# Optimization experiments

Hardware: AMD Instinct MI355X
Metric: run time of the kernel (lower is better)

The kernel has to match this reference:

```python
import jax, jax.numpy as jnp
import numpy as np

# Module hyperparameters (init_kwargs): d_in=256, d_out=512, nh=8 -> dv=dk=dd=64
D_IN, D_OUT, NH = 256, 512, 8
DV = D_OUT // NH   # 64
DK = DV            # 64
DD = DK            # 64
KH, KW = 3, 7
D_HID = NH * DK + DK + DV  # 640 (kernel_type='VplusR')
EPS = 1e-6


def l2norm(x, axis):
    # matches torch: x / sqrt(sum(x^2) + eps)
    return x / jnp.sqrt(jnp.sum(x * x, axis=axis, keepdims=True) + EPS)


def conv_same(x, w, groups=1):
    # x: NHWC, w: HWIO, 'same' padding matching torch pad=(KH//2, KW//2)
    return jax.lax.conv_general_dilated(
        x, w, window_strides=(1, 1),
        padding=((KH // 2, KH // 2), (KW // 2, KW // 2)),
        dimension_numbers=('NHWC', 'HWIO', 'NHWC'),
        feature_group_count=groups)


def setup_inputs() -> dict:
    key = jax.random.key(0)
    ks = jax.random.split(key, 8)
    x = jax.random.normal(ks[0], (8, 64, 32, D_IN), jnp.float32)  # [N, T, H, C]
    # projection_linear: two bias-free Linears (torch weight [out, in])
    W1 = jax.random.normal(ks[1], (D_HID, D_IN), jnp.float32) / np.sqrt(D_IN)
    W2 = jax.random.normal(ks[2], (D_HID, D_HID), jnp.float32) / np.sqrt(D_HID)
    # P1 init: randn(dk, dd) * sqrt(1/(ksize*dd))
    P1 = jax.random.normal(ks[3], (DK, DD), jnp.float32) * np.sqrt(1.0 / (KH * KW * DD))
    # H1: grouped Conv2d(dk, dk*dd, groups=dk) -> HWIO weight (KH, KW, 1, DK*DD)
    H1_w = jax.random.normal(ks[4], (KH, KW, 1, DK * DD), jnp.float32) / np.sqrt(KH * KW)
    # H2: Conv2d(1, dd) -> (KH, KW, 1, DD)
    H2_w = jax.random.normal(ks[5], (KH, KW, 1, DD), jnp.float32) / np.sqrt(KH * KW)
    # G: Conv2d(1, dv) -> (KH, KW, 1, DV)
    G_w = jax.random.normal(ks[6], (KH, KW, 1, DV), jnp.float32) / np.sqrt(KH * KW)
    I = jnp.eye(DK, dtype=jnp.float32)  # self.I parameter (identity init)
    return {"x": x, "W1": W1, "W2": W2, "P1": P1,
            "H1_w": H1_w, "H2_w": H2_w, "G_w": G_w, "I": I}


def reference(x, W1, W2, P1, H1_w, H2_w, G_w, I):
    b, T, H, _ = x.shape
    # projection_linear: Linear -> SiLU -> Linear on channel dim
    xp = jax.nn.silu(x @ W1.T) @ W2.T                      # [b,T,H,d_hid]
    q = xp[..., : NH * DK].reshape(b, T, H, NH, DK)        # 'b t h (nh k)'
    k = xp[..., NH * DK : NH * DK + DK]                    # [b,T,H,DK]
    v = xp[..., NH * DK + DK :]                            # [b,T,H,DV]
    q = l2norm(q, axis=-1)
    k = l2norm(k, axis=-1)
    v = l2norm(v, axis=-1)
    # H1: grouped depthwise-style conv generating per-pixel dk x dd kernels
    K_H1 = conv_same(k, H1_w, groups=DK).reshape(b, T, H, DK, DD) + P1
    # kernel = einsum over dk: [b,T,H,NH,DD]
    kernel = jnp.einsum('bthnk,bthkd->bthnd', q, K_H1)
    # H2 / G applied independently to each of the DV channels of v (shared weights):
    # torch treats (b v) as batch with 1 channel; equivalent grouped conv with tiled weight.
    V = conv_same(v, jnp.tile(H2_w, (1, 1, 1, DV)), groups=DV).reshape(b, T, H, DV, DD)
    V_G = conv_same(v, jnp.tile(G_w, (1, 1, 1, DV)), groups=DV).reshape(b, T, H, DV, DV) + I
    # feature = einsum('abc,abd->acd', V_G, V): contract over first dv index
    feature = jnp.einsum('bthvc,bthvd->bthcd', V_G, V)     # [b,T,H,DV,DD]
    # out = einsum('abc,adc->adb', kernel, feature): [bth, DV, NH]
    out = jnp.einsum('bthnd,bthvd->bthvn', kernel, feature)
    # rearrange '(b t h) nh v -> b (nh v) t h' then permute back -> [b,T,H,DV*NH]
    return out.reshape(b, T, H, DV * NH)
```

## Files before the change

### kernel.cpp

```cpp
#include <hip/hip_runtime.h>
#include <hip/hip_bf16.h>

#define NPIX 16384

using short8 = __attribute__((ext_vector_type(8))) short;
using half8  = __attribute__((ext_vector_type(8))) _Float16;
using half4  = __attribute__((ext_vector_type(4))) _Float16;
using half2v = __attribute__((ext_vector_type(2))) _Float16;
using f32x4  = __attribute__((ext_vector_type(4))) float;

__device__ inline short bf16s(float x) {
  __hip_bfloat16 b = __float2bfloat16(x);
  return *reinterpret_cast<short*>(&b);
}

__global__ __launch_bounds__(256) void prep_all(const float* __restrict__ W1,
                                                const float* __restrict__ W2,
                                                const float* __restrict__ H1w,
                                                const float* __restrict__ P1,
                                                const float* __restrict__ H2w,
                                                __hip_bfloat16* __restrict__ W1_bf,
                                                __hip_bfloat16* __restrict__ W2_bf,
                                                _Float16* __restrict__ Wt,
                                                _Float16* __restrict__ H2h) {
  int i = blockIdx.x * 256 + threadIdx.x;
  const int n1 = 640 * 256, n2 = 640 * 640, n3 = 64 * 1408;
  if (i < n1) {
    W1_bf[i] = __float2bfloat16(W1[i]);
  } else if (i < n1 + n2) {
    W2_bf[i - n1] = __float2bfloat16(W2[i - n1]);
  } else if (i < n1 + n2 + n3) {
    int j = i - n1 - n2;
    int dd = j & 63, k = j >> 6;
    float v;
    if (k < 1344) { int t = k >> 6, c = k & 63; v = H1w[t * 4096 + c * 64 + dd]; }
    else          { int c = k - 1344;          v = P1[c * 64 + dd]; }
    Wt[(size_t)dd * 1408 + k] = (_Float16)v;
  } else if (i < n1 + n2 + n3 + 2048) {
    int j = i - n1 - n2 - n3;
    int t = j >> 6, dd = j & 63;
    H2h[j] = (t < 21) ? (_Float16)H2w[t * 64 + dd] : (_Float16)0.f;
  }
}

template<int K>
__global__ __launch_bounds__(256) void gemm_st(const float* __restrict__ Af,
                                               const short* __restrict__ B,
                                               __hip_bfloat16* __restrict__ Cb) {
  __shared__ short As[2][128][36];
  __shared__ short Bs[2][128][36];
  const int tid = threadIdx.x, lane = tid & 63, wid = tid >> 6;
  const int row0 = blockIdx.y * 128, col0 = blockIdx.x * 128;
  const int sr = tid >> 1, sc = (tid & 1) * 16;
  const int l15 = lane & 15, lk = (lane >> 4) * 8;
  const int wr = (wid >> 1) * 64, wc = (wid & 1) * 64;
  const int NS = K / 32;

  short8 aL, aH, bL, bH;
  auto loadTile = [&](int s) {
    const float* src = Af + (size_t)(row0 + sr) * K + s * 32 + sc;
    float4 f0 = *(const float4*)(src);
    float4 f1 = *(const float4*)(src + 4);
    float4 f2 = *(const float4*)(src + 8);
    float4 f3 = *(const float4*)(src + 12);
    aL[0] = bf16s(f0.x); aL[1] = bf16s(f0.y); aL[2] = bf16s(f0.z); aL[3] = bf16s(f0.w);
    aL[4] = bf16s(f1.x); aL[5] = bf16s(f1.y); aL[6] = bf16s(f1.z); aL[7] = bf16s(f1.w);
    aH[0] = bf16s(f2.x); aH[1] = bf16s(f2.y); aH[2] = bf16s(f2.z); aH[3] = bf16s(f2.w);
    aH[4] = bf16s(f3.x); aH[5] = bf16s(f3.y); aH[6] = bf16s(f3.z); aH[7] = bf16s(f3.w);
    const short* srcB = B + (size_t)(col0 + sr) * K + s * 32 + sc;
    bL = *(const short8*)srcB;
    bH = *(const short8*)(srcB + 8);
  };
  auto writeTile = [&](int buf) {
    *(short8*)&As[buf][sr][sc]     = aL;
    *(short8*)&As[buf][sr][sc + 8] = aH;
    *(short8*)&Bs[buf][sr][sc]     = bL;
    *(short8*)&Bs[buf][sr][sc + 8] = bH;
  };

  loadTile(0);
  writeTile(0);
  __syncthreads();

  f32x4 acc[4][4];
#pragma unroll
  for (int mi = 0; mi < 4; ++mi)
#pragma unroll
    for (int nj = 0; nj < 4; ++nj) acc[mi][nj] = (f32x4){0.f, 0.f, 0.f, 0.f};

  for (int s = 0; s < NS; ++s) {
    const int cur = s & 1;
    if (s + 1 < NS) loadTile(s + 1);
    short8 af[4], bfr[4];
#pragma unroll
    for (int mi = 0; mi < 4; ++mi)
      af[mi] = *(const short8*)&As[cur][wr + mi * 16 + l15][lk];
#pragma unroll
    for (int nj = 0; nj < 4; ++nj)
      bfr[nj] = *(const short8*)&Bs[cur][wc + nj * 16 + l15][lk];
#pragma unroll
    for (int mi = 0; mi < 4; ++mi)
#pragma unroll
      for (int nj = 0; nj < 4; ++nj)
        acc[mi][nj] = __builtin_amdgcn_mfma_f32_16x16x32_bf16(af[mi], bfr[nj], acc[mi][nj], 0, 0, 0);
    if (s + 1 < NS) writeTile(cur ^ 1);
    __syncthreads();
  }

  const int r0 = (lane >> 4) * 4;
#pragma unroll
  for (int mi = 0; mi < 4; ++mi)
#pragma unroll
    for (int nj = 0; nj < 4; ++nj)
#pragma unroll
      for (int r = 0; r < 4; ++r) {
        int row = row0 + wr + mi * 16 + r0 + r;
        int col = col0 + wc + nj * 16 + l15;
        float v = acc[mi][nj][r];
        v = v / (1.f + __expf(-v));
        Cb[(size_t)row * 640 + col] = __float2bfloat16(v);
      }
}

__global__ __launch_bounds__(256) void gemm_qkv(const short* __restrict__ Ab,
                                                const short* __restrict__ B,
                                                _Float16* __restrict__ qn,
                                                _Float16* __restrict__ kn,
                                                _Float16* __restrict__ vn) {
  __shared__ short As[2][128][36];
  __shared__ short Bs[2][128][36];
  const int tid = threadIdx.x, lane = tid & 63, wid = tid >> 6;
  const int row0 = blockIdx.y * 128, col0 = blockIdx.x * 128;
  const int sr = tid >> 1, sc = (tid & 1) * 16;
  const int l15 = lane & 15, lk = (lane >> 4) * 8;
  const int wr = (wid >> 1) * 64, wc = (wid & 1) * 64;
  const int NS = 20;

  short8 aL, aH, bL, bH;
  auto loadTile = [&](int s) {
    const short* src = Ab + (size_t)(row0 + sr) * 640 + s * 32 + sc;
    aL = *(const short8*)src;
    aH = *(const short8*)(src + 8);
    const short* srcB = B + (size_t)(col0 + sr) * 640 + s * 32 + sc;
    bL = *(const short8*)srcB;
    bH = *(const short8*)(srcB + 8);
  };
  auto writeTile = [&](int buf) {
    *(short8*)&As[buf][sr][sc]     = aL;
    *(short8*)&As[buf][sr][sc + 8] = aH;
    *(short8*)&Bs[buf][sr][sc]     = bL;
    *(short8*)&Bs[buf][sr][sc + 8] = bH;
  };

  loadTile(0);
  writeTile(0);
  __syncthreads();

  f32x4 acc[4][4];
#pragma unroll
  for (int mi = 0; mi < 4; ++mi)
#pragma unroll
    for (int nj = 0; nj < 4; ++nj) acc[mi][nj] = (f32x4){0.f, 0.f, 0.f, 0.f};

  for (int s = 0; s < NS; ++s) {
    const int cur = s & 1;
    if (s + 1 < NS) loadTile(s + 1);
    short8 af[4], bfr[4];
#pragma unroll
    for (int mi = 0; mi < 4; ++mi)
      af[mi] = *(const short8*)&As[cur][wr + mi * 16 + l15][lk];
#pragma unroll
    for (int nj = 0; nj < 4; ++nj)
      bfr[nj] = *(const short8*)&Bs[cur][wc + nj * 16 + l15][lk];
#pragma unroll
    for (int mi = 0; mi < 4; ++mi)
#pragma unroll
      for (int nj = 0; nj < 4; ++nj)
        acc[mi][nj] = __builtin_amdgcn_mfma_f32_16x16x32_bf16(af[mi], bfr[nj], acc[mi][nj], 0, 0, 0);
    if (s + 1 < NS) writeTile(cur ^ 1);
    __syncthreads();
  }

  const int r0g = (lane >> 4) * 4;
  const int ct = blockIdx.x;
  const int colh = wid & 1;
#pragma unroll
  for (int mi = 0; mi < 4; ++mi)
#pragma unroll
    for (int r = 0; r < 4; ++r) {
      float s = 0.f;
#pragma unroll
      for (int nj = 0; nj < 4; ++nj) s += acc[mi][nj][r] * acc[mi][nj][r];
      s += __shfl_xor(s, 1); s += __shfl_xor(s, 2);
      s += __shfl_xor(s, 4); s += __shfl_xor(s, 8);
      float inv = 1.f / sqrtf(s + 1e-6f);
      int row = row0 + wr + mi * 16 + r0g + r;
      _Float16* dst;
      if (ct < 4) dst = qn + (size_t)row * 512 + (ct * 2 + colh) * 64;
      else        dst = (colh == 0 ? kn : vn) + (size_t)row * 64;
#pragma unroll
      for (int nj = 0; nj < 4; ++nj)
        dst[nj * 16 + l15] = (_Float16)(acc[mi][nj][r] * inv);
    }
}

__global__ __launch_bounds__(256, 4) void fused_kp(const _Float16* __restrict__ qn_g,
                                                   const _Float16* __restrict__ kn,
                                                   const _Float16* __restrict__ vn,
                                                   const _Float16* __restrict__ Wt,
                                                   const _Float16* __restrict__ H2h,
                                                   const float* __restrict__ Gw,
                                                   float* __restrict__ out) {
  __shared__ _Float16 qn_s[128][72];
  __shared__ _Float16 win[66][72];
  __shared__ _Float16 Bt[2][64][40];

  float*    Zs  = (float*)&qn_s[0][0];
  _Float16* ZMs = (_Float16*)((char*)&qn_s[0][0] + 10752);
  _Float16* Gt  = &Bt[0][0][0];
  _Float16* GwS = &Bt[0][0][0] + 2576;

  int tid = threadIdx.x, lane = tid & 63, wid = tid >> 6;
  int pb = blockIdx.x * 16;
  int h0 = pb & 31, t0 = (pb >> 5) & 63, batch = pb >> 11;
  const int sd = tid >> 2, skq = (tid & 3) * 8;
  const int rt0 = wid * 2;
  const int l15 = lane & 15, lk = (lane >> 4) * 8;

  half8 q00, q01, q10, q11;
  int pix0, pix1;
  {
    int grow0 = (rt0 + 0) * 16 + l15;
    int grow1 = (rt0 + 1) * 16 + l15;
    pix0 = grow0 >> 3; pix1 = grow1 >> 3;
    const _Float16* b = qn_g + (size_t)pb * 512;
    q00 = *(const half8*)(b + grow0 * 64 + lk);
    q01 = *(const half8*)(b + grow0 * 64 + 32 + lk);
    q10 = *(const half8*)(b + grow1 * 64 + lk);
    q11 = *(const half8*)(b + grow1 * 64 + 32 + lk);
  }

  for (int idx = tid; idx < 528; idx += 256) {
    int j = idx >> 3, c0 = (idx & 7) * 8;
    int dy = j / 22, hx = j % 22;
    int t = t0 - 1 + dy, h = h0 - 3 + hx;
    half8 v = {0, 0, 0, 0, 0, 0, 0, 0};
    if ((unsigned)t < 64u && (unsigned)h < 32u)
      v = *(const half8*)(kn + ((size_t)((batch * 64 + t) * 32 + h)) * 64 + c0);
    *(half8*)&win[j][c0] = v;
  }
  *(half8*)&Bt[0][sd][skq] = *(const half8*)(Wt + (size_t)sd * 1408 + skq);
  __syncthreads();

  f32x4 acc[2][4];
#pragma unroll
  for (int rt = 0; rt < 2; ++rt)
#pragma unroll
    for (int nj = 0; nj < 4; ++nj) acc[rt][nj] = (f32x4){0.f, 0.f, 0.f, 0.f};

  for (int ss = 0; ss < 22; ++ss) {
    const int sA = ss * 2, sB = sA + 1;
    const int dy = ss / 7, dxx = ss % 7;

    {
      half8 stage = *(const half8*)(Wt + (size_t)sd * 1408 + (sA + 1) * 32 + skq);
      half8 bfr[4];
#pragma unroll
      for (int nj = 0; nj < 4; ++nj)
        bfr[nj] = *(const half8*)&Bt[0][nj * 16 + l15][lk];
      half8 a0, a1;
      if (ss < 21) {
        a0 = q00 * *(const half8*)&win[dy * 22 + pix0 + dxx][lk];
        a1 = q10 * *(const half8*)&win[dy * 22 + pix1 + dxx][lk];
      } else {
        a0 = q00; a1 = q10;
      }
#pragma unroll
      for (int nj = 0; nj < 4; ++nj) {
        acc[0][nj] = __builtin_amdgcn_mfma_f32_16x16x32_f16(a0, bfr[nj], acc[0][nj], 0, 0, 0);
        acc[1][nj] = __builtin_amdgcn_mfma_f32_16x16x32_f16(a1, bfr[nj], acc[1][nj], 0, 0, 0);
      }
      *(half8*)&Bt[1][sd][skq] = stage;
      __syncthreads();
    }
    {
      half8 stage;
      if (sB < 43)
        stage = *(const half8*)(Wt + (size_t)sd * 1408 + (sB + 1) * 32 + skq);
      half8 bfr[4];
#pragma unroll
      for (int nj = 0; nj < 4; ++nj)
        bfr[nj] = *(const half8*)&Bt[1][nj * 16 + l15][lk];
      half8 a0, a1;
      if (ss < 21) {
        a0 = q01 * *(const half8*)&win[dy * 22 + pix0 + dxx][32 + lk];
        a1 = q11 * *(const half8*)&win[dy * 22 + pix1 + dxx][32 + lk];
      } else {
        a0 = q01; a1 = q11;
      }
#pragma unroll
      for (int nj = 0; nj < 4; ++nj) {
        acc[0][nj] = __builtin_amdgcn_mfma_f32_16x16x32_f16(a0, bfr[nj], acc[0][nj], 0, 0, 0);
        acc[1][nj] = __builtin_amdgcn_mfma_f32_16x16x32_f16(a1, bfr[nj], acc[1][nj], 0, 0, 0);
      }
      if (sB < 43) *(half8*)&Bt[0][sd][skq] = stage;
      __syncthreads();
    }
  }

  _Float16* kld = &qn_s[0][0];
  const int r0 = (lane >> 4) * 4;
#pragma unroll
  for (int rt = 0; rt < 2; ++rt) {
    int growb = (rt0 + rt) * 16;
#pragma unroll
    for (int nj = 0; nj < 4; ++nj)
#pragma unroll
      for (int r = 0; r < 4; ++r)
        kld[(growb + r0 + r) * 72 + nj * 16 + l15] = (_Float16)acc[rt][nj][r];
  }

  f32x4 accZ[2][2];
#pragma unroll
  for (int rt = 0; rt < 2; ++rt)
#pragma unroll
    for (int ct = 0; ct < 2; ++ct) accZ[rt][ct] = (f32x4){0.f, 0.f, 0.f, 0.f};
#pragma unroll
  for (int k2 = 0; k2 < 2; ++k2) {
    half8 bz[2];
#pragma unroll
    for (int ct = 0; ct < 2; ++ct)
      bz[ct] = *(const half8*)(H2h + (ct * 16 + l15) * 64 + k2 * 32 + lk);
#pragma unroll
    for (int rt = 0; rt < 2; ++rt) {
      half8 az = *(const half8*)&kld[((rt0 + rt) * 16 + l15) * 72 + k2 * 32 + lk];
#pragma unroll
      for (int ct = 0; ct < 2; ++ct)
        accZ[rt][ct] = __builtin_amdgcn_mfma_f32_16x16x32_f16(az, bz[ct], accZ[rt][ct], 0, 0, 0);
    }
  }
  __syncthreads();

#pragma unroll
  for (int rt = 0; rt < 2; ++rt)
#pragma unroll
    for (int ct = 0; ct < 2; ++ct) {
      int t = ct * 16 + l15;
      if (t < 21) {
#pragma unroll
        for (int r = 0; r < 4; ++r) {
          int grow = (rt0 + rt) * 16 + r0 + r;
          Zs[((grow >> 3) * 21 + t) * 8 + (grow & 7)] = accZ[rt][ct][r];
        }
      }
    }
  for (int idx = tid; idx < 528; idx += 256) {
    int j = idx >> 3, c0 = (idx & 7) * 8;
    int dy = j / 22, hx = j % 22;
    int t = t0 - 1 + dy, h = h0 - 3 + hx;
    half8 v = {0, 0, 0, 0, 0, 0, 0, 0};
    if ((unsigned)t < 64u && (unsigned)h < 32u)
      v = *(const half8*)(vn + ((size_t)((batch * 64 + t) * 32 + h)) * 64 + c0);
    *(half8*)&win[j][c0] = v;
  }
  for (int idx = tid; idx < 168; idx += 256) {
    int t = idx >> 3, c0 = (idx & 7) * 8;
    const float* g = Gw + t * 64 + c0;
    half8 o;
#pragma unroll
    for (int j = 0; j < 8; ++j) o[j] = (_Float16)g[j];
    *(half8*)&GwS[t * 64 + c0] = o;
  }
  __syncthreads();

  {
    const half8 hz = {0, 0, 0, 0, 0, 0, 0, 0};
    int c = 0;
#pragma unroll
    for (int ti = 0; ti < 5; ++ti)
#pragma unroll
      for (int tj = ti; tj < 5; ++tj, ++c) {
        if ((c & 3) == wid) {
          f32x4 g = {0.f, 0.f, 0.f, 0.f};
          const int ra = ti * 16 + l15, rb = tj * 16 + l15;
#pragma unroll
          for (int k2 = 0; k2 < 2; ++k2) {
            half8 av = (ra < 66) ? *(const half8*)&win[ra][k2 * 32 + lk] : hz;
            half8 bv = (rb < 66) ? *(const half8*)&win[rb][k2 * 32 + lk] : hz;
            g = __builtin_amdgcn_mfma_f32_16x16x32_f16(av, bv, g, 0, 0, 0);
          }
#pragma unroll
          for (int r = 0; r < 4; ++r) {
            int j1 = ti * 16 + r0 + r, j2 = tj * 16 + l15;
            if (j1 < 66 && j2 < 66) {
              int dy1 = j1 / 22, x1 = j1 % 22;
              int dy2 = j2 / 22, x2 = j2 % 22;
              int d = x2 - x1 + 6;
              _Float16 val = (_Float16)g[r];
              if ((unsigned)d < 13u)
                Gt[(dy1 * 3 + dy2) * 286 + x1 * 13 + d] = val;
              if (ti != tj) {
                int d2 = 12 - d;
                if ((unsigned)d2 < 13u)
                  Gt[(dy2 * 3 + dy1) * 286 + x2 * 13 + d2] = val;
              }
            }
          }
        }
      }
  }
  __syncthreads();

  for (int task = tid; task < 336; task += 256) {
    int pix = task / 21, t1 = task % 21;
    int dy1 = t1 / 7, dx1i = t1 % 7;
    int x1 = pix + dx1i;
    f32x4 s0 = {0.f, 0.f, 0.f, 0.f}, s1 = {0.f, 0.f, 0.f, 0.f};
#pragma unroll
    for (int t2 = 0; t2 < 21; ++t2) {
      float m = (float)Gt[(dy1 * 3 + t2 / 7) * 286 + x1 * 13 + (t2 % 7) - dx1i + 6];
      s0 += m * *(const f32x4*)&Zs[(pix * 21 + t2) * 8];
      s1 += m * *(const f32x4*)&Zs[(pix * 21 + t2) * 8 + 4];
    }
    half4 lo = {(_Float16)s0[0], (_Float16)s0[1], (_Float16)s0[2], (_Float16)s0[3]};
    half4 hi = {(_Float16)s1[0], (_Float16)s1[1], (_Float16)s1[2], (_Float16)s1[3]};
    *(half4*)&ZMs[(pix * 21 + t1) * 8]     = lo;
    *(half4*)&ZMs[(pix * 21 + t1) * 8 + 4] = hi;
  }
  __syncthreads();

  for (int task = tid; task < 512; task += 256) {
    int pix = task >> 5, v0 = (task & 31) * 2;
    f32x4 a0[2] = {{0.f,0.f,0.f,0.f},{0.f,0.f,0.f,0.f}};
    f32x4 a1[2] = {{0.f,0.f,0.f,0.f},{0.f,0.f,0.f,0.f}};
#pragma unroll
    for (int t = 0; t < 21; ++t) {
      half2v sv = *(const half2v*)&win[(t / 7) * 22 + pix + (t % 7)][v0];
      half2v gw = *(const half2v*)&GwS[t * 64 + v0];
      f32x4 z0 = *(const f32x4*)&Zs[(pix * 21 + t) * 8];
      f32x4 z1 = *(const f32x4*)&Zs[(pix * 21 + t) * 8 + 4];
      half8 zm = *(const half8*)&ZMs[(pix * 21 + t) * 8];
      f32x4 m0 = {(float)zm[0], (float)zm[1], (float)zm[2], (float)zm[3]};
      f32x4 m1 = {(float)zm[4], (float)zm[5], (float)zm[6], (float)zm[7]};
#pragma unroll
      for (int j = 0; j < 2; ++j) {
        float svf = (float)sv[j], gwf = (float)gw[j];
        a0[j] += svf * z0 + gwf * m0;
        a1[j] += svf * z1 + gwf * m1;
      }
    }
#pragma unroll
    for (int j = 0; j < 2; ++j) {
      float* dst = out + (size_t)(pb + pix) * 512 + (v0 + j) * 8;
      *(f32x4*)dst = a0[j];
      *(f32x4*)(dst + 4) = a1[j];
    }
  }
}

extern "C" void kernel_launch(void* const* d_in, const int* in_sizes, int n_in,
                              void* d_out, int out_size, void* d_ws, size_t ws_size,
                              hipStream_t stream) {
  const float* x   = (const float*)d_in[0];
  const float* W1  = (const float*)d_in[1];
  const float* W2  = (const float*)d_in[2];
  const float* P1  = (const float*)d_in[3];
  const float* H1w = (const float*)d_in[4];
  const float* H2w = (const float*)d_in[5];
  const float* Gw  = (const float*)d_in[6];
  float* out = (float*)d_out;

  char* ws = (char*)d_ws;
  __hip_bfloat16* h_bf = (__hip_bfloat16*)(ws);
  _Float16* qn         = (_Float16*)(ws + 20971520);
  _Float16* kn         = (_Float16*)(ws + 37748736);
  _Float16* vn         = (_Float16*)(ws + 39845888);
  __hip_bfloat16* W1_bf= (__hip_bfloat16*)(ws + 41943040);
  __hip_bfloat16* W2_bf= (__hip_bfloat16*)(ws + 42270720);
  _Float16* Wt         = (_Float16*)(ws + 43089920);
  _Float16* H2h        = (_Float16*)(ws + 43270144);

  prep_all<<<dim3(2600), dim3(256), 0, stream>>>(W1, W2, H1w, P1, H2w,
                                                 W1_bf, W2_bf, Wt, H2h);

  gemm_st<256><<<dim3(5, 128), dim3(256), 0, stream>>>(x, (const short*)W1_bf, h_bf);
  gemm_qkv<<<dim3(5, 128), dim3(256), 0, stream>>>(
      (const short*)h_bf, (const short*)W2_bf, qn, kn, vn);

  fused_kp<<<dim3(NPIX / 16), dim3(256), 0, stream>>>(qn, kn, vn, Wt, H2h, Gw, out);
}
```

Measured before the change: 119.7 us.

## Load Wt MFMA B-fragments directly from global into registers, removing LDS staging and barriers

```diff
diff --git a/kernel.cpp b/kernel.cpp
--- a/kernel.cpp
+++ b/kernel.cpp
@@ -213,17 +213,16 @@
                                                    float* __restrict__ out) {
   __shared__ _Float16 qn_s[128][72];
   __shared__ _Float16 win[66][72];
-  __shared__ _Float16 Bt[2][64][40];
+  __shared__ _Float16 gtbuf[3920];
 
   float*    Zs  = (float*)&qn_s[0][0];
   _Float16* ZMs = (_Float16*)((char*)&qn_s[0][0] + 10752);
-  _Float16* Gt  = &Bt[0][0][0];
-  _Float16* GwS = &Bt[0][0][0] + 2576;
+  _Float16* Gt  = &gtbuf[0];
+  _Float16* GwS = &gtbuf[2576];
 
   int tid = threadIdx.x, lane = tid & 63, wid = tid >> 6;
   int pb = blockIdx.x * 16;
   int h0 = pb & 31, t0 = (pb >> 5) & 63, batch = pb >> 11;
-  const int sd = tid >> 2, skq = (tid & 3) * 8;
   const int rt0 = wid * 2;
   const int l15 = lane & 15, lk = (lane >> 4) * 8;
 
@@ -240,6 +239,11 @@
     q11 = *(const half8*)(b + grow1 * 64 + 32 + lk);
   }
 
+  const _Float16* wrow0 = Wt + (size_t)(0 * 16 + l15) * 1408 + lk;
+  const _Float16* wrow1 = Wt + (size_t)(1 * 16 + l15) * 1408 + lk;
+  const _Float16* wrow2 = Wt + (size_t)(2 * 16 + l15) * 1408 + lk;
+  const _Float16* wrow3 = Wt + (size_t)(3 * 16 + l15) * 1408 + lk;
+
   for (int idx = tid; idx < 528; idx += 256) {
     int j = idx >> 3, c0 = (idx & 7) * 8;
     int dy = j / 22, hx = j % 22;
@@ -249,7 +253,14 @@
       v = *(const half8*)(kn + ((size_t)((batch * 64 + t) * 32 + h)) * 64 + c0);
     *(half8*)&win[j][c0] = v;
   }
-  *(half8*)&Bt[0][sd][skq] = *(const half8*)(Wt + (size_t)sd * 1408 + skq);
+  half8 bfA0 = *(const half8*)(wrow0);
+  half8 bfA1 = *(const half8*)(wrow1);
+  half8 bfA2 = *(const half8*)(wrow2);
+  half8 bfA3 = *(const half8*)(wrow3);
+  half8 bfB0 = *(const half8*)(wrow0 + 32);
+  half8 bfB1 = *(const half8*)(wrow1 + 32);
+  half8 bfB2 = *(const half8*)(wrow2 + 32);
+  half8 bfB3 = *(const half8*)(wrow3 + 32);
   __syncthreads();
 
   f32x4 acc[2][4];
@@ -263,11 +274,6 @@
     const int dy = ss / 7, dxx = ss % 7;
 
     {
-      half8 stage = *(const half8*)(Wt + (size_t)sd * 1408 + (sA + 1) * 32 + skq);
-      half8 bfr[4];
-#pragma unroll
-      for (int nj = 0; nj < 4; ++nj)
-        bfr[nj] = *(const half8*)&Bt[0][nj * 16 + l15][lk];
       half8 a0, a1;
       if (ss < 21) {
         a0 = q00 * *(const half8*)&win[dy * 22 + pix0 + dxx][lk];
@@ -275,22 +281,23 @@
       } else {
         a0 = q00; a1 = q10;
       }
-#pragma unroll
-      for (int nj = 0; nj < 4; ++nj) {
-        acc[0][nj] = __builtin_amdgcn_mfma_f32_16x16x32_f16(a0, bfr[nj], acc[0][nj], 0, 0, 0);
-        acc[1][nj] = __builtin_amdgcn_mfma_f32_16x16x32_f16(a1, bfr[nj], acc[1][nj], 0, 0, 0);
-      }
-      *(half8*)&Bt[1][sd][skq] = stage;
-      __syncthreads();
+      acc[0][0] = __builtin_amdgcn_mfma_f32_16x16x32_f16(a0, bfA0, acc[0][0], 0, 0, 0);
+      acc[0][1] = __builtin_amdgcn_mfma_f32_16x16x32_f16(a0, bfA1, acc[0][1], 0, 0, 0);
+      acc[0][2] = __builtin_amdgcn_mfma_f32_16x16x32_f16(a0, bfA2, acc[0][2], 0, 0, 0);
+      acc[0][3] = __builtin_amdgcn_mfma_f32_16x16x32_f16(a0, bfA3, acc[0][3], 0, 0, 0);
+      acc[1][0] = __builtin_amdgcn_mfma_f32_16x16x32_f16(a1, bfA0, acc[1][0], 0, 0, 0);
+      acc[1][1] = __builtin_amdgcn_mfma_f32_16x16x32_f16(a1, bfA1, acc[1][1], 0, 0, 0);
+      acc[1][2] = __builtin_amdgcn_mfma_f32_16x16x32_f16(a1, bfA2, acc[1][2], 0, 0, 0);
+      acc[1][3] = __builtin_amdgcn_mfma_f32_16x16x32_f16(a1, bfA3, acc[1][3], 0, 0, 0);
+      if (sA + 2 < 44) {
+        const int c = (sA + 2) * 32;
+        bfA0 = *(const half8*)(wrow0 + c);
+        bfA1 = *(const half8*)(wrow1 + c);
+        bfA2 = *(const half8*)(wrow2 + c);
+        bfA3 = *(const half8*)(wrow3 + c);
+      }
     }
     {
-      half8 stage;
-      if (sB < 43)
-        stage = *(const half8*)(Wt + (size_t)sd * 1408 + (sB + 1) * 32 + skq);
-      half8 bfr[4];
-#pragma unroll
-      for (int nj = 0; nj < 4; ++nj)
-        bfr[nj] = *(const half8*)&Bt[1][nj * 16 + l15][lk];
       half8 a0, a1;
       if (ss < 21) {
         a0 = q01 * *(const half8*)&win[dy * 22 + pix0 + dxx][32 + lk];
@@ -298,13 +305,21 @@
       } else {
         a0 = q01; a1 = q11;
       }
-#pragma unroll
-      for (int nj = 0; nj < 4; ++nj) {
-        acc[0][nj] = __builtin_amdgcn_mfma_f32_16x16x32_f16(a0, bfr[nj], acc[0][nj], 0, 0, 0);
-        acc[1][nj] = __builtin_amdgcn_mfma_f32_16x16x32_f16(a1, bfr[nj], acc[1][nj], 0, 0, 0);
-      }
-      if (sB < 43) *(half8*)&Bt[0][sd][skq] = stage;
-      __syncthreads();
+      acc[0][0] = __builtin_amdgcn_mfma_f32_16x16x32_f16(a0, bfB0, acc[0][0], 0, 0, 0);
+      acc[0][1] = __builtin_amdgcn_mfma_f32_16x16x32_f16(a0, bfB1, acc[0][1], 0, 0, 0);
+      acc[0][2] = __builtin_amdgcn_mfma_f32_16x16x32_f16(a0, bfB2, acc[0][2], 0, 0, 0);
+      acc[0][3] = __builtin_amdgcn_mfma_f32_16x16x32_f16(a0, bfB3, acc[0][3], 0, 0, 0);
+      acc[1][0] = __builtin_amdgcn_mfma_f32_16x16x32_f16(a1, bfB0, acc[1][0], 0, 0, 0);
+      acc[1][1] = __builtin_amdgcn_mfma_f32_16x16x32_f16(a1, bfB1, acc[1][1], 0, 0, 0);
+      acc[1][2] = __builtin_amdgcn_mfma_f32_16x16x32_f16(a1, bfB2, acc[1][2], 0, 0, 0);
+      acc[1][3] = __builtin_amdgcn_mfma_f32_16x16x32_f16(a1, bfB3, acc[1][3], 0, 0, 0);
+      if (sB + 2 < 44) {
+        const int c = (sB + 2) * 32;
+        bfB0 = *(const half8*)(wrow0 + c);
+        bfB1 = *(const half8*)(wrow1 + c);
+        bfB2 = *(const half8*)(wrow2 + c);
+        bfB3 = *(const half8*)(wrow3 + c);
+      }
     }
   }
 
```

Result: slower. 166.0 us (+38.7%).
